# Performance work log

Measured on AMD Instinct MI355X. Metric: run time of the kernel, lower is better.

## Reference

```python
import jax, jax.numpy as jnp
import numpy as np

DIM = 1024

def setup_inputs() -> dict:
    key = jax.random.key(0)
    ks = jax.random.split(key, 7)
    s = 1.0 / np.sqrt(DIM)  # roughly match nn.Linear init scale
    return {
        "x": jax.random.normal(ks[0], (4, 2048, DIM), dtype=jnp.float32),
        "Wq": jax.random.normal(ks[1], (DIM, DIM), dtype=jnp.float32) * s,
        "bq": jax.random.normal(ks[2], (DIM,), dtype=jnp.float32) * s,
        "Wk": jax.random.normal(ks[3], (DIM, DIM), dtype=jnp.float32) * s,
        "bk": jax.random.normal(ks[4], (DIM,), dtype=jnp.float32) * s,
        "Wv": jax.random.normal(ks[5], (DIM, DIM), dtype=jnp.float32) * s,
        "bv": jax.random.normal(ks[6], (DIM,), dtype=jnp.float32) * s,
    }

def reference(x, Wq, bq, Wk, bk, Wv, bv):
    # torch Linear: y = x @ W.T + b
    C = x.shape[-1]
    scale = C ** (-0.5)
    q = jnp.einsum('bnc,dc->bnd', x, Wq) + bq
    k = jnp.einsum('bnc,dc->bnd', x, Wk) + bk
    v = jnp.einsum('bnc,dc->bnd', x, Wv) + bv
    attn = jnp.einsum('bnd,bmd->bnm', q, k) * scale  # [B,N,N]
    attn = jax.nn.softmax(attn, axis=-1)
    out = jnp.einsum('bnm,bmd->bnd', attn, v)
    return out
```

## Files before the change

kernel.cpp:

```cpp
#include <hip/hip_runtime.h>

#define SEQ  2048
#define DIM  1024
#define NTOK 8192
#define NQKV 3072

typedef __attribute__((ext_vector_type(8))) __bf16 bf16x8;
typedef __attribute__((ext_vector_type(4))) float  f32x4;

__device__ __forceinline__ unsigned short f2bf(float f) {
    unsigned int u = __float_as_uint(f);
    u += 0x7fffu + ((u >> 16) & 1u);
    return (unsigned short)(u >> 16);
}

__device__ __forceinline__ float bfu2f(unsigned int lo16) {
    return __uint_as_float(lo16 << 16);
}

__device__ __forceinline__ void load_lds_128(const unsigned short* g, unsigned short* l) {
    __builtin_amdgcn_global_load_lds(
        (const __attribute__((address_space(1))) void*)g,
        (__attribute__((address_space(3))) void*)l, 16, 0, 0);
}

#define BAR() asm volatile("s_barrier" ::: "memory")

template <int MODE>
__global__ __launch_bounds__(512, 2)
void gemm256(const unsigned short* __restrict__ A, const unsigned short* __restrict__ B,
             void* __restrict__ Cv,
             const float* __restrict__ b0v, const float* __restrict__ b1v,
             const float* __restrict__ b2v, unsigned short* __restrict__ vt,
             const float* __restrict__ inv_rs,
             int K, int lda, int ldb, int ldc,
             long sA, long sB, long sC, float alpha)
{
    constexpr int AT = 256 * 64;
    constexpr int BT = 128 * 64;
    __shared__ __align__(16) unsigned short As[3 * AT];
    __shared__ __align__(16) unsigned short Bs[3 * BT];

    const int tid  = threadIdx.x;
    const int wave = tid >> 6;
    const int lane = tid & 63;
    const int l4   = lane & 15;
    const int lh   = lane >> 4;
    const int wm   = wave >> 1;
    const int wn   = wave & 1;

    const int m0 = blockIdx.x * 256;
    const int n0 = blockIdx.y * 128;
    const int z  = blockIdx.z;
    A += (long)z * sA;
    B += (long)z * sB;

    const int r0 = tid >> 3;
    const int gc = (tid & 7) ^ (r0 & 7);
    const unsigned short* Ag = A + (long)(m0 + r0) * lda + gc * 8;
    const unsigned short* Bg = B + (long)(n0 + r0) * ldb + gc * 8;
    unsigned short* Al = As + tid * 8;
    unsigned short* Bl = Bs + tid * 8;

    const int NT = K >> 6;

    auto stage = [&](int t, int slot, int ph) {
        const long kof = (long)t * 64;
        unsigned short* al = Al + slot * AT;
        unsigned short* bl = Bl + slot * BT;
        if (ph == 0) {
            load_lds_128(Ag + kof,                          al);
            load_lds_128(Ag + kof + (long)64 * lda,         al + 4096);
            load_lds_128(Bg + kof,                          bl);
        } else {
            load_lds_128(Ag + kof + (long)128 * lda,        al + 8192);
            load_lds_128(Ag + kof + (long)192 * lda,        al + 12288);
            load_lds_128(Bg + kof + (long)64 * ldb,         bl + 4096);
        }
    };

    const int aoff = (wm * 64 + l4) * 64;
    const int boff = (wn * 64 + l4) * 64;
    const int cs0  = ((0 + lh) ^ (lane & 7)) * 8;
    const int cs1  = ((4 + lh) ^ (lane & 7)) * 8;

    f32x4 acc[4][4] = {};
    bf16x8 a0[4], b0[4], a1[4], b1[4];

    auto ldfrag = [&](bf16x8 (&a)[4], bf16x8 (&b)[4],
                      const unsigned short* Ab, const unsigned short* Bb, int cs) {
#pragma unroll
        for (int mf = 0; mf < 4; ++mf) a[mf] = *(const bf16x8*)(Ab + mf * 1024 + cs);
#pragma unroll
        for (int nf = 0; nf < 4; ++nf) b[nf] = *(const bf16x8*)(Bb + nf * 1024 + cs);
    };
    auto mfma16 = [&](bf16x8 (&a)[4], bf16x8 (&b)[4]) {
        __builtin_amdgcn_s_setprio(1);
#pragma unroll
        for (int mf = 0; mf < 4; ++mf)
#pragma unroll
            for (int nf = 0; nf < 4; ++nf)
                acc[mf][nf] = __builtin_amdgcn_mfma_f32_16x16x32_bf16(
                    a[mf], b[nf], acc[mf][nf], 0, 0, 0);
        __builtin_amdgcn_s_setprio(0);
    };

    stage(0, 0, 0); stage(0, 0, 1);
    stage(1, 1, 0); stage(1, 1, 1);
    asm volatile("s_waitcnt vmcnt(6)" ::: "memory");
    BAR();
    ldfrag(a0, b0, As + aoff, Bs + boff, cs0);

    int sl = 0;
    for (int t = 0; t < NT; ++t) {
        const unsigned short* Ab = As + sl * AT + aoff;
        const unsigned short* Bb = Bs + sl * BT + boff;
        const int st  = (sl >= 1) ? sl - 1 : 2;
        const int nsl = (sl == 2) ? 0 : sl + 1;

        ldfrag(a1, b1, Ab, Bb, cs1);
        if (t + 2 < NT) stage(t + 2, st, 0);
        mfma16(a0, b0);

        if (t + 2 < NT) stage(t + 2, st, 1);
        asm volatile("s_waitcnt lgkmcnt(0)" ::: "memory");
        if (t < NT - 2) asm volatile("s_waitcnt vmcnt(6)" ::: "memory");
        else            asm volatile("s_waitcnt vmcnt(0)" ::: "memory");
        BAR();
        if (t + 1 < NT)
            ldfrag(a0, b0, As + nsl * AT + aoff, Bs + nsl * BT + boff, cs0);
        mfma16(a1, b1);
        sl = nsl;
    }

    const int r0c = m0 + wm * 64 + lh * 4;
    const int c0c = n0 + wn * 64 + l4;

    if (MODE == 0) {
        if (n0 >= 2048) {
#pragma unroll
            for (int nf = 0; nf < 4; ++nf) {
                const int d = c0c + nf * 16 - 2048;
                const float bias = b2v[d];
#pragma unroll
                for (int mf = 0; mf < 4; ++mf) {
                    const int row = r0c + mf * 16;
                    const int bb = row >> 11;
                    const int mm = row & 2047;
                    ushort4 u;
                    u.x = f2bf(acc[mf][nf][0] + bias);
                    u.y = f2bf(acc[mf][nf][1] + bias);
                    u.z = f2bf(acc[mf][nf][2] + bias);
                    u.w = f2bf(acc[mf][nf][3] + bias);
                    *(ushort4*)(vt + ((long)bb * DIM + d) * SEQ + mm) = u;
                }
            }
        } else {
            unsigned short* C16 = (unsigned short*)Cv;
#pragma unroll
            for (int nf = 0; nf < 4; ++nf) {
                const int col = c0c + nf * 16;
                const float bias = (col >= 1024) ? b1v[col - 1024] : b0v[col];
#pragma unroll
                for (int mf = 0; mf < 4; ++mf)
#pragma unroll
                    for (int r = 0; r < 4; ++r)
                        C16[(long)(r0c + mf * 16 + r) * ldc + col] =
                            f2bf(acc[mf][nf][r] + bias);
            }
        }
    } else if (MODE == 1) {
        float* C = (float*)Cv + (long)z * sC;
        const float* ir = inv_rs + (long)z * SEQ;
#pragma unroll
        for (int mf = 0; mf < 4; ++mf) {
            const int row = r0c + mf * 16;
            const float4 inv4 = *(const float4*)(ir + row);
#pragma unroll
            for (int nf = 0; nf < 4; ++nf) {
                const int col = c0c + nf * 16;
                C[(long)(row + 0) * ldc + col] = acc[mf][nf][0] * inv4.x;
                C[(long)(row + 1) * ldc + col] = acc[mf][nf][1] * inv4.y;
                C[(long)(row + 2) * ldc + col] = acc[mf][nf][2] * inv4.z;
                C[(long)(row + 3) * ldc + col] = acc[mf][nf][3] * inv4.w;
            }
        }
    } else {
        unsigned short* C16 = (unsigned short*)Cv + (long)z * sC;
#pragma unroll
        for (int nf = 0; nf < 4; ++nf) {
            const int col = c0c + nf * 16;
#pragma unroll
            for (int mf = 0; mf < 4; ++mf)
#pragma unroll
                for (int r = 0; r < 4; ++r)
                    C16[(long)(r0c + mf * 16 + r) * ldc + col] =
                        f2bf(__expf(acc[mf][nf][r] * alpha));
        }
    }
}

__global__ __launch_bounds__(256)
void cvt_x(const float* __restrict__ src, unsigned short* __restrict__ dst, int n4)
{
    int i = blockIdx.x * 256 + threadIdx.x;
    if (i < n4) {
        float4 f = ((const float4*)src)[i];
        ushort4 u;
        u.x = f2bf(f.x); u.y = f2bf(f.y); u.z = f2bf(f.z); u.w = f2bf(f.w);
        ((ushort4*)dst)[i] = u;
    }
}

__global__ __launch_bounds__(256)
void cvt_w3(const float* __restrict__ Wq, const float* __restrict__ Wk,
            const float* __restrict__ Wv, unsigned short* __restrict__ dst)
{
    const int sel = blockIdx.y;
    const float* src = (sel == 0) ? Wq : ((sel == 1) ? Wk : Wv);
    const int i = blockIdx.x * 256 + threadIdx.x;
    float4 f = ((const float4*)src)[i];
    ushort4 u;
    u.x = f2bf(f.x); u.y = f2bf(f.y); u.z = f2bf(f.z); u.w = f2bf(f.w);
    ((ushort4*)(dst + (long)sel * DIM * DIM))[i] = u;
}

__global__ __launch_bounds__(256)
void rowsum_inv(const unsigned short* __restrict__ P, float* __restrict__ inv_rs)
{
    const int row  = blockIdx.x * 4 + (threadIdx.x >> 6);
    const int lane = threadIdx.x & 63;
    const unsigned short* pr = P + (long)row * SEQ;

    float s = 0.f;
#pragma unroll
    for (int it = 0; it < 4; ++it) {
        uint4 u = *(const uint4*)(pr + (it * 64 + lane) * 8);
        s += bfu2f(u.x & 0xffffu) + __uint_as_float(u.x & 0xffff0000u);
        s += bfu2f(u.y & 0xffffu) + __uint_as_float(u.y & 0xffff0000u);
        s += bfu2f(u.z & 0xffffu) + __uint_as_float(u.z & 0xffff0000u);
        s += bfu2f(u.w & 0xffffu) + __uint_as_float(u.w & 0xffff0000u);
    }
    for (int off = 32; off > 0; off >>= 1)
        s += __shfl_xor(s, off);
    if (lane == 0) inv_rs[row] = 1.0f / s;
}

extern "C" void kernel_launch(void* const* d_in, const int* in_sizes, int n_in,
                              void* d_out, int out_size, void* d_ws, size_t ws_size,
                              hipStream_t stream)
{
    const float* x  = (const float*)d_in[0];
    const float* Wq = (const float*)d_in[1];
    const float* bq = (const float*)d_in[2];
    const float* Wk = (const float*)d_in[3];
    const float* bk = (const float*)d_in[4];
    const float* Wv = (const float*)d_in[5];
    const float* bv = (const float*)d_in[6];
    float* out = (float*)d_out;

    char* ws = (char*)d_ws;
    unsigned short* xb   = (unsigned short*)ws;
    unsigned short* Wb   = (unsigned short*)(ws + 16u * 1024 * 1024);
    unsigned short* qkv  = (unsigned short*)(ws + 64u * 1024 * 1024);
    unsigned short* vt   = (unsigned short*)(ws + 112u * 1024 * 1024);
    unsigned short* P    = (unsigned short*)(ws + 128u * 1024 * 1024);
    float*          irs  = (float*)(ws + 160u * 1024 * 1024);

    const float scale = 0.03125f;
    dim3 blk(256);
    dim3 blk512(512);

    cvt_x<<<NTOK * DIM / 4 / 256, blk, 0, stream>>>(x, xb, NTOK * DIM / 4);
    cvt_w3<<<dim3(DIM * DIM / 4 / 256, 3), blk, 0, stream>>>(Wq, Wk, Wv, Wb);

    gemm256<0><<<dim3(NTOK / 256, NQKV / 128), blk512, 0, stream>>>(
        xb, Wb, qkv, bq, bk, bv, vt, nullptr,
        DIM, DIM, DIM, NQKV, 0, 0, 0, 1.0f);

    gemm256<2><<<dim3(SEQ / 256, SEQ / 128, 4), blk512, 0, stream>>>(
        qkv, qkv + 1024, P, nullptr, nullptr, nullptr, nullptr, nullptr,
        DIM, NQKV, NQKV, SEQ,
        (long)SEQ * NQKV, (long)SEQ * NQKV, (long)SEQ * SEQ, scale);

    rowsum_inv<<<NTOK / 4, blk, 0, stream>>>(P, irs);

    gemm256<1><<<dim3(SEQ / 256, DIM / 128, 4), blk512, 0, stream>>>(
        P, vt, out, nullptr, nullptr, nullptr, nullptr, irs,
        SEQ, SEQ, SEQ, DIM,
        (long)SEQ * SEQ, (long)DIM * SEQ, (long)SEQ * DIM, 1.0f);
}
```

Before: 244.0 us.

## Enlarge GEMM tiles to 256-wide N with 2x4 wave grid and double buffering

Replaces the 256x128 triple-buffered GEMM with a templated kernel using 256-column N tiles, a 2x4 wave layout, and a variable M tile (256 or 128). Each K-step now loads both k-halves of the fragments at once and issues the MFMAs in four quadrant groups. The aim is more operand reuse per LDS byte and fewer blocks per GEMM. In exchange, the finer-grained phased prefetch is replaced by a simple double buffer that waits for all loads every iteration. That may expose memory latency and raise register pressure.

```diff
diff --git a/kernel.cpp b/kernel.cpp
--- a/kernel.cpp
+++ b/kernel.cpp
@@ -26,31 +26,33 @@
 
 #define BAR() asm volatile("s_barrier" ::: "memory")
 
-template <int MODE>
+template <int MODE, int MB>
 __global__ __launch_bounds__(512, 2)
-void gemm256(const unsigned short* __restrict__ A, const unsigned short* __restrict__ B,
-             void* __restrict__ Cv,
-             const float* __restrict__ b0v, const float* __restrict__ b1v,
-             const float* __restrict__ b2v, unsigned short* __restrict__ vt,
-             const float* __restrict__ inv_rs,
-             int K, int lda, int ldb, int ldc,
-             long sA, long sB, long sC, float alpha)
-{
-    constexpr int AT = 256 * 64;
-    constexpr int BT = 128 * 64;
-    __shared__ __align__(16) unsigned short As[3 * AT];
-    __shared__ __align__(16) unsigned short Bs[3 * BT];
+void gemm2(const unsigned short* __restrict__ A, const unsigned short* __restrict__ B,
+           void* __restrict__ Cv,
+           const float* __restrict__ b0v, const float* __restrict__ b1v,
+           const float* __restrict__ b2v, unsigned short* __restrict__ vt,
+           const float* __restrict__ inv_rs,
+           int K, int lda, int ldb, int ldc,
+           long sA, long sB, long sC, float alpha)
+{
+    constexpr int BM = MB * 128;
+    constexpr int AT = BM * 64;
+    constexpr int BT = 256 * 64;
+    constexpr int MH = MB * 2;
+    __shared__ __align__(16) unsigned short As[2 * AT];
+    __shared__ __align__(16) unsigned short Bs[2 * BT];
 
     const int tid  = threadIdx.x;
     const int wave = tid >> 6;
     const int lane = tid & 63;
     const int l4   = lane & 15;
     const int lh   = lane >> 4;
-    const int wm   = wave >> 1;
-    const int wn   = wave & 1;
-
-    const int m0 = blockIdx.x * 256;
-    const int n0 = blockIdx.y * 128;
+    const int wm   = wave >> 2;
+    const int wn   = wave & 3;
+
+    const int m0 = blockIdx.x * BM;
+    const int n0 = blockIdx.y * 256;
     const int z  = blockIdx.z;
     A += (long)z * sA;
     B += (long)z * sB;
@@ -64,76 +66,97 @@
 
     const int NT = K >> 6;
 
-    auto stage = [&](int t, int slot, int ph) {
+    auto stage = [&](int t, int u) {
         const long kof = (long)t * 64;
-        unsigned short* al = Al + slot * AT;
-        unsigned short* bl = Bl + slot * BT;
-        if (ph == 0) {
-            load_lds_128(Ag + kof,                          al);
-            load_lds_128(Ag + kof + (long)64 * lda,         al + 4096);
-            load_lds_128(Bg + kof,                          bl);
-        } else {
-            load_lds_128(Ag + kof + (long)128 * lda,        al + 8192);
-            load_lds_128(Ag + kof + (long)192 * lda,        al + 12288);
-            load_lds_128(Bg + kof + (long)64 * ldb,         bl + 4096);
-        }
+#pragma unroll
+        for (int p = 0; p < 2 * MB; ++p)
+            load_lds_128(Ag + kof + (long)(64 * p) * lda, Al + u * AT + p * 4096);
+#pragma unroll
+        for (int p = 0; p < 4; ++p)
+            load_lds_128(Bg + kof + (long)(64 * p) * ldb, Bl + u * BT + p * 4096);
     };
 
-    const int aoff = (wm * 64 + l4) * 64;
+    const int aoff = (wm * (BM / 2) + l4) * 64;
     const int boff = (wn * 64 + l4) * 64;
     const int cs0  = ((0 + lh) ^ (lane & 7)) * 8;
     const int cs1  = ((4 + lh) ^ (lane & 7)) * 8;
 
-    f32x4 acc[4][4] = {};
-    bf16x8 a0[4], b0[4], a1[4], b1[4];
-
-    auto ldfrag = [&](bf16x8 (&a)[4], bf16x8 (&b)[4],
-                      const unsigned short* Ab, const unsigned short* Bb, int cs) {
-#pragma unroll
-        for (int mf = 0; mf < 4; ++mf) a[mf] = *(const bf16x8*)(Ab + mf * 1024 + cs);
-#pragma unroll
-        for (int nf = 0; nf < 4; ++nf) b[nf] = *(const bf16x8*)(Bb + nf * 1024 + cs);
-    };
-    auto mfma16 = [&](bf16x8 (&a)[4], bf16x8 (&b)[4]) {
+    f32x4 acc[4 * MB][4] = {};
+    bf16x8 alo[MH][2], ahi[MH][2], bfr[4][2];
+
+    stage(0, 0);
+    asm volatile("s_waitcnt vmcnt(0)" ::: "memory");
+    BAR();
+
+    for (int t = 0; t < NT; ++t) {
+        const int u = t & 1;
+        const unsigned short* Ab = As + u * AT + aoff;
+        const unsigned short* Bb = Bs + u * BT + boff;
+
+        if (t + 1 < NT) stage(t + 1, u ^ 1);
+
+#pragma unroll
+        for (int nf = 0; nf < 4; ++nf) {
+            bfr[nf][0] = *(const bf16x8*)(Bb + nf * 1024 + cs0);
+            bfr[nf][1] = *(const bf16x8*)(Bb + nf * 1024 + cs1);
+        }
+#pragma unroll
+        for (int mf = 0; mf < MH; ++mf) {
+            alo[mf][0] = *(const bf16x8*)(Ab + mf * 1024 + cs0);
+            alo[mf][1] = *(const bf16x8*)(Ab + mf * 1024 + cs1);
+        }
+#pragma unroll
+        for (int mf = 0; mf < MH; ++mf) {
+            ahi[mf][0] = *(const bf16x8*)(Ab + (MH + mf) * 1024 + cs0);
+            ahi[mf][1] = *(const bf16x8*)(Ab + (MH + mf) * 1024 + cs1);
+        }
+
         __builtin_amdgcn_s_setprio(1);
 #pragma unroll
-        for (int mf = 0; mf < 4; ++mf)
-#pragma unroll
-            for (int nf = 0; nf < 4; ++nf)
-                acc[mf][nf] = __builtin_amdgcn_mfma_f32_16x16x32_bf16(
-                    a[mf], b[nf], acc[mf][nf], 0, 0, 0);
+        for (int mf = 0; mf < MH; ++mf)
+#pragma unroll
+            for (int nf = 0; nf < 2; ++nf)
+#pragma unroll
+                for (int kk = 0; kk < 2; ++kk)
+                    acc[mf][nf] = __builtin_amdgcn_mfma_f32_16x16x32_bf16(
+                        alo[mf][kk], bfr[nf][kk], acc[mf][nf], 0, 0, 0);
         __builtin_amdgcn_s_setprio(0);
-    };
-
-    stage(0, 0, 0); stage(0, 0, 1);
-    stage(1, 1, 0); stage(1, 1, 1);
-    asm volatile("s_waitcnt vmcnt(6)" ::: "memory");
-    BAR();
-    ldfrag(a0, b0, As + aoff, Bs + boff, cs0);
-
-    int sl = 0;
-    for (int t = 0; t < NT; ++t) {
-        const unsigned short* Ab = As + sl * AT + aoff;
-        const unsigned short* Bb = Bs + sl * BT + boff;
-        const int st  = (sl >= 1) ? sl - 1 : 2;
-        const int nsl = (sl == 2) ? 0 : sl + 1;
-
-        ldfrag(a1, b1, Ab, Bb, cs1);
-        if (t + 2 < NT) stage(t + 2, st, 0);
-        mfma16(a0, b0);
-
-        if (t + 2 < NT) stage(t + 2, st, 1);
-        asm volatile("s_waitcnt lgkmcnt(0)" ::: "memory");
-        if (t < NT - 2) asm volatile("s_waitcnt vmcnt(6)" ::: "memory");
-        else            asm volatile("s_waitcnt vmcnt(0)" ::: "memory");
+        __builtin_amdgcn_s_setprio(1);
+#pragma unroll
+        for (int mf = 0; mf < MH; ++mf)
+#pragma unroll
+            for (int nf = 2; nf < 4; ++nf)
+#pragma unroll
+                for (int kk = 0; kk < 2; ++kk)
+                    acc[mf][nf] = __builtin_amdgcn_mfma_f32_16x16x32_bf16(
+                        alo[mf][kk], bfr[nf][kk], acc[mf][nf], 0, 0, 0);
+        __builtin_amdgcn_s_setprio(0);
+        __builtin_amdgcn_s_setprio(1);
+#pragma unroll
+        for (int mf = 0; mf < MH; ++mf)
+#pragma unroll
+            for (int nf = 2; nf < 4; ++nf)
+#pragma unroll
+                for (int kk = 0; kk < 2; ++kk)
+                    acc[MH + mf][nf] = __builtin_amdgcn_mfma_f32_16x16x32_bf16(
+                        ahi[mf][kk], bfr[nf][kk], acc[MH + mf][nf], 0, 0, 0);
+        __builtin_amdgcn_s_setprio(0);
+        __builtin_amdgcn_s_setprio(1);
+#pragma unroll
+        for (int mf = 0; mf < MH; ++mf)
+#pragma unroll
+            for (int nf = 0; nf < 2; ++nf)
+#pragma unroll
+                for (int kk = 0; kk < 2; ++kk)
+                    acc[MH + mf][nf] = __builtin_amdgcn_mfma_f32_16x16x32_bf16(
+                        ahi[mf][kk], bfr[nf][kk], acc[MH + mf][nf], 0, 0, 0);
+        __builtin_amdgcn_s_setprio(0);
+
+        asm volatile("s_waitcnt vmcnt(0) lgkmcnt(0)" ::: "memory");
         BAR();
-        if (t + 1 < NT)
-            ldfrag(a0, b0, As + nsl * AT + aoff, Bs + nsl * BT + boff, cs0);
-        mfma16(a1, b1);
-        sl = nsl;
     }
 
-    const int r0c = m0 + wm * 64 + lh * 4;
+    const int r0c = m0 + wm * (BM / 2) + lh * 4;
     const int c0c = n0 + wn * 64 + l4;
 
     if (MODE == 0) {
@@ -143,7 +166,7 @@
                 const int d = c0c + nf * 16 - 2048;
                 const float bias = b2v[d];
 #pragma unroll
-                for (int mf = 0; mf < 4; ++mf) {
+                for (int mf = 0; mf < 4 * MB; ++mf) {
                     const int row = r0c + mf * 16;
                     const int bb = row >> 11;
                     const int mm = row & 2047;
@@ -162,7 +185,7 @@
                 const int col = c0c + nf * 16;
                 const float bias = (col >= 1024) ? b1v[col - 1024] : b0v[col];
 #pragma unroll
-                for (int mf = 0; mf < 4; ++mf)
+                for (int mf = 0; mf < 4 * MB; ++mf)
 #pragma unroll
                     for (int r = 0; r < 4; ++r)
                         C16[(long)(r0c + mf * 16 + r) * ldc + col] =
@@ -173,7 +196,7 @@
         float* C = (float*)Cv + (long)z * sC;
         const float* ir = inv_rs + (long)z * SEQ;
 #pragma unroll
-        for (int mf = 0; mf < 4; ++mf) {
+        for (int mf = 0; mf < 4 * MB; ++mf) {
             const int row = r0c + mf * 16;
             const float4 inv4 = *(const float4*)(ir + row);
 #pragma unroll
@@ -191,7 +214,7 @@
         for (int nf = 0; nf < 4; ++nf) {
             const int col = c0c + nf * 16;
 #pragma unroll
-            for (int mf = 0; mf < 4; ++mf)
+            for (int mf = 0; mf < 4 * MB; ++mf)
 #pragma unroll
                 for (int r = 0; r < 4; ++r)
                     C16[(long)(r0c + mf * 16 + r) * ldc + col] =
@@ -274,18 +297,18 @@
     cvt_x<<<NTOK * DIM / 4 / 256, blk, 0, stream>>>(x, xb, NTOK * DIM / 4);
     cvt_w3<<<dim3(DIM * DIM / 4 / 256, 3), blk, 0, stream>>>(Wq, Wk, Wv, Wb);
 
-    gemm256<0><<<dim3(NTOK / 256, NQKV / 128), blk512, 0, stream>>>(
+    gemm2<0, 2><<<dim3(NTOK / 256, NQKV / 256), blk512, 0, stream>>>(
         xb, Wb, qkv, bq, bk, bv, vt, nullptr,
         DIM, DIM, DIM, NQKV, 0, 0, 0, 1.0f);
 
-    gemm256<2><<<dim3(SEQ / 256, SEQ / 128, 4), blk512, 0, stream>>>(
+    gemm2<2, 2><<<dim3(SEQ / 256, SEQ / 256, 4), blk512, 0, stream>>>(
         qkv, qkv + 1024, P, nullptr, nullptr, nullptr, nullptr, nullptr,
         DIM, NQKV, NQKV, SEQ,
         (long)SEQ * NQKV, (long)SEQ * NQKV, (long)SEQ * SEQ, scale);
 
     rowsum_inv<<<NTOK / 4, blk, 0, stream>>>(P, irs);
 
-    gemm256<1><<<dim3(SEQ / 256, DIM / 128, 4), blk512, 0, stream>>>(
+    gemm2<1, 1><<<dim3(SEQ / 128, DIM / 256, 4), blk512, 0, stream>>>(
         P, vt, out, nullptr, nullptr, nullptr, nullptr, irs,
         SEQ, SEQ, SEQ, DIM,
         (long)SEQ * SEQ, (long)DIM * SEQ, (long)SEQ * DIM, 1.0f);
```

Measured after the change: 272.9 us. +11.8%, slower.

## Fuse softmax row-sum into QK^T epilogue and add smaller-tile PV GEMM

Applied to the files above, without the earlier changes.

The QK^T exp epilogue now accumulates bf16-rounded row sums with shuffles and atomicAdd into a zeroed buffer. This removes the separate rowsum pass that re-read the whole P matrix. The PV product moves to a new 128x128-tile kernel with double buffering and higher occupancy, which divides by the row sum in its epilogue. The atomics add contention and an extra zeroing launch, and the smaller tiles lower reuse in exchange for more blocks.

```diff
diff --git a/kernel.cpp b/kernel.cpp
--- a/kernel.cpp
+++ b/kernel.cpp
@@ -32,7 +32,7 @@
              void* __restrict__ Cv,
              const float* __restrict__ b0v, const float* __restrict__ b1v,
              const float* __restrict__ b2v, unsigned short* __restrict__ vt,
-             const float* __restrict__ inv_rs,
+             float* __restrict__ rsv,
              int K, int lda, int ldb, int ldc,
              long sA, long sB, long sC, float alpha)
 {
@@ -169,33 +169,138 @@
                             f2bf(acc[mf][nf][r] + bias);
             }
         }
-    } else if (MODE == 1) {
-        float* C = (float*)Cv + (long)z * sC;
-        const float* ir = inv_rs + (long)z * SEQ;
-#pragma unroll
-        for (int mf = 0; mf < 4; ++mf) {
-            const int row = r0c + mf * 16;
-            const float4 inv4 = *(const float4*)(ir + row);
-#pragma unroll
-            for (int nf = 0; nf < 4; ++nf) {
-                const int col = c0c + nf * 16;
-                C[(long)(row + 0) * ldc + col] = acc[mf][nf][0] * inv4.x;
-                C[(long)(row + 1) * ldc + col] = acc[mf][nf][1] * inv4.y;
-                C[(long)(row + 2) * ldc + col] = acc[mf][nf][2] * inv4.z;
-                C[(long)(row + 3) * ldc + col] = acc[mf][nf][3] * inv4.w;
-            }
-        }
     } else {
         unsigned short* C16 = (unsigned short*)Cv + (long)z * sC;
-#pragma unroll
-        for (int nf = 0; nf < 4; ++nf) {
-            const int col = c0c + nf * 16;
-#pragma unroll
-            for (int mf = 0; mf < 4; ++mf)
-#pragma unroll
-                for (int r = 0; r < 4; ++r)
-                    C16[(long)(r0c + mf * 16 + r) * ldc + col] =
-                        f2bf(__expf(acc[mf][nf][r] * alpha));
+        float* rs = rsv + (long)z * SEQ;
+#pragma unroll
+        for (int mf = 0; mf < 4; ++mf)
+#pragma unroll
+            for (int r = 0; r < 4; ++r) {
+                const int rowi = r0c + mf * 16 + r;
+                float s = 0.f;
+#pragma unroll
+                for (int nf = 0; nf < 4; ++nf) {
+                    const int col = c0c + nf * 16;
+                    const unsigned short pu = f2bf(__expf(acc[mf][nf][r] * alpha));
+                    C16[(long)rowi * ldc + col] = pu;
+                    s += bfu2f(pu);
+                }
+                s += __shfl_xor(s, 1);
+                s += __shfl_xor(s, 2);
+                s += __shfl_xor(s, 4);
+                s += __shfl_xor(s, 8);
+                if (l4 == 0) atomicAdd(rs + rowi, s);
+            }
+    }
+}
+
+__global__ __launch_bounds__(512, 4)
+void gemm_pv(const unsigned short* __restrict__ A, const unsigned short* __restrict__ B,
+             float* __restrict__ C, const float* __restrict__ rsv,
+             int K, int lda, int ldb, int ldc, long sA, long sB, long sC)
+{
+    constexpr int AT = 128 * 64;
+    constexpr int BT = 128 * 64;
+    __shared__ __align__(16) unsigned short As[2 * AT];
+    __shared__ __align__(16) unsigned short Bs[2 * BT];
+
+    const int tid  = threadIdx.x;
+    const int wave = tid >> 6;
+    const int lane = tid & 63;
+    const int l4   = lane & 15;
+    const int lh   = lane >> 4;
+    const int wm   = wave >> 2;
+    const int wn   = wave & 3;
+
+    const int m0 = blockIdx.x * 128;
+    const int n0 = blockIdx.y * 128;
+    const int z  = blockIdx.z;
+    A += (long)z * sA;
+    B += (long)z * sB;
+
+    const int r0 = tid >> 3;
+    const int gc = (tid & 7) ^ (r0 & 7);
+    const unsigned short* Ag = A + (long)(m0 + r0) * lda + gc * 8;
+    const unsigned short* Bg = B + (long)(n0 + r0) * ldb + gc * 8;
+    unsigned short* Al = As + tid * 8;
+    unsigned short* Bl = Bs + tid * 8;
+
+    const int NT = K >> 6;
+
+    auto stage = [&](int t, int u) {
+        const long kof = (long)t * 64;
+        load_lds_128(Ag + kof,                  Al + u * AT);
+        load_lds_128(Ag + kof + (long)64 * lda, Al + u * AT + 4096);
+        load_lds_128(Bg + kof,                  Bl + u * BT);
+        load_lds_128(Bg + kof + (long)64 * ldb, Bl + u * BT + 4096);
+    };
+
+    const int aoff = (wm * 64 + l4) * 64;
+    const int boff = (wn * 32 + l4) * 64;
+    const int cs0  = (lh ^ (lane & 7)) * 8;
+    const int cs1  = ((4 + lh) ^ (lane & 7)) * 8;
+
+    f32x4 acc[4][2] = {};
+    bf16x8 aR[4][2], bR[2][2];
+
+    stage(0, 0);
+    asm volatile("s_waitcnt vmcnt(0)" ::: "memory");
+    BAR();
+
+    for (int t = 0; t < NT; ++t) {
+        const int u = t & 1;
+        const unsigned short* Ab = As + u * AT + aoff;
+        const unsigned short* Bb = Bs + u * BT + boff;
+
+        if (t + 1 < NT) stage(t + 1, u ^ 1);
+
+#pragma unroll
+        for (int mf = 0; mf < 4; ++mf) {
+            aR[mf][0] = *(const bf16x8*)(Ab + mf * 1024 + cs0);
+            aR[mf][1] = *(const bf16x8*)(Ab + mf * 1024 + cs1);
+        }
+#pragma unroll
+        for (int n = 0; n < 2; ++n) {
+            bR[n][0] = *(const bf16x8*)(Bb + n * 1024 + cs0);
+            bR[n][1] = *(const bf16x8*)(Bb + n * 1024 + cs1);
+        }
+
+        __builtin_amdgcn_s_setprio(1);
+#pragma unroll
+        for (int mf = 0; mf < 4; ++mf)
+#pragma unroll
+            for (int n = 0; n < 2; ++n)
+                acc[mf][n] = __builtin_amdgcn_mfma_f32_16x16x32_bf16(
+                    aR[mf][0], bR[n][0], acc[mf][n], 0, 0, 0);
+#pragma unroll
+        for (int mf = 0; mf < 4; ++mf)
+#pragma unroll
+            for (int n = 0; n < 2; ++n)
+                acc[mf][n] = __builtin_amdgcn_mfma_f32_16x16x32_bf16(
+                    aR[mf][1], bR[n][1], acc[mf][n], 0, 0, 0);
+        __builtin_amdgcn_s_setprio(0);
+
+        asm volatile("s_waitcnt vmcnt(0) lgkmcnt(0)" ::: "memory");
+        BAR();
+    }
+
+    float* Cz = C + (long)z * sC;
+    const float* rs = rsv + (long)z * SEQ;
+    const int r0c = m0 + wm * 64 + lh * 4;
+    const int c0c = n0 + wn * 32 + l4;
+#pragma unroll
+    for (int mf = 0; mf < 4; ++mf) {
+        const int rowb = r0c + mf * 16;
+        const float4 rs4 = *(const float4*)(rs + rowb);
+        const float i0 = 1.0f / rs4.x, i1 = 1.0f / rs4.y;
+        const float i2 = 1.0f / rs4.z, i3 = 1.0f / rs4.w;
+#pragma unroll
+        for (int n = 0; n < 2; ++n) {
+            const int col = c0c + n * 16;
+            Cz[(long)(rowb + 0) * ldc + col] = acc[mf][n][0] * i0;
+            Cz[(long)(rowb + 1) * ldc + col] = acc[mf][n][1] * i1;
+            Cz[(long)(rowb + 2) * ldc + col] = acc[mf][n][2] * i2;
+            Cz[(long)(rowb + 3) * ldc + col] = acc[mf][n][3] * i3;
         }
     }
 }
@@ -226,24 +331,9 @@
 }
 
 __global__ __launch_bounds__(256)
-void rowsum_inv(const unsigned short* __restrict__ P, float* __restrict__ inv_rs)
-{
-    const int row  = blockIdx.x * 4 + (threadIdx.x >> 6);
-    const int lane = threadIdx.x & 63;
-    const unsigned short* pr = P + (long)row * SEQ;
-
-    float s = 0.f;
-#pragma unroll
-    for (int it = 0; it < 4; ++it) {
-        uint4 u = *(const uint4*)(pr + (it * 64 + lane) * 8);
-        s += bfu2f(u.x & 0xffffu) + __uint_as_float(u.x & 0xffff0000u);
-        s += bfu2f(u.y & 0xffffu) + __uint_as_float(u.y & 0xffff0000u);
-        s += bfu2f(u.z & 0xffffu) + __uint_as_float(u.z & 0xffff0000u);
-        s += bfu2f(u.w & 0xffffu) + __uint_as_float(u.w & 0xffff0000u);
-    }
-    for (int off = 32; off > 0; off >>= 1)
-        s += __shfl_xor(s, off);
-    if (lane == 0) inv_rs[row] = 1.0f / s;
+void zero_rs(float* __restrict__ rs)
+{
+    rs[blockIdx.x * 256 + threadIdx.x] = 0.f;
 }
 
 extern "C" void kernel_launch(void* const* d_in, const int* in_sizes, int n_in,
@@ -265,7 +355,7 @@
     unsigned short* qkv  = (unsigned short*)(ws + 64u * 1024 * 1024);
     unsigned short* vt   = (unsigned short*)(ws + 112u * 1024 * 1024);
     unsigned short* P    = (unsigned short*)(ws + 128u * 1024 * 1024);
-    float*          irs  = (float*)(ws + 160u * 1024 * 1024);
+    float*          rs   = (float*)(ws + 160u * 1024 * 1024);
 
     const float scale = 0.03125f;
     dim3 blk(256);
@@ -273,20 +363,19 @@
 
     cvt_x<<<NTOK * DIM / 4 / 256, blk, 0, stream>>>(x, xb, NTOK * DIM / 4);
     cvt_w3<<<dim3(DIM * DIM / 4 / 256, 3), blk, 0, stream>>>(Wq, Wk, Wv, Wb);
+    zero_rs<<<NTOK / 256, blk, 0, stream>>>(rs);
 
     gemm256<0><<<dim3(NTOK / 256, NQKV / 128), blk512, 0, stream>>>(
         xb, Wb, qkv, bq, bk, bv, vt, nullptr,
         DIM, DIM, DIM, NQKV, 0, 0, 0, 1.0f);
 
     gemm256<2><<<dim3(SEQ / 256, SEQ / 128, 4), blk512, 0, stream>>>(
-        qkv, qkv + 1024, P, nullptr, nullptr, nullptr, nullptr, nullptr,
+        qkv, qkv + 1024, P, nullptr, nullptr, nullptr, nullptr, rs,
         DIM, NQKV, NQKV, SEQ,
         (long)SEQ * NQKV, (long)SEQ * NQKV, (long)SEQ * SEQ, scale);
 
-    rowsum_inv<<<NTOK / 4, blk, 0, stream>>>(P, irs);
-
-    gemm256<1><<<dim3(SEQ / 256, DIM / 128, 4), blk512, 0, stream>>>(
-        P, vt, out, nullptr, nullptr, nullptr, nullptr, irs,
+    gemm_pv<<<dim3(SEQ / 128, DIM / 128, 4), blk512, 0, stream>>>(
+        P, vt, out, rs,
         SEQ, SEQ, SEQ, DIM,
-        (long)SEQ * SEQ, (long)DIM * SEQ, (long)SEQ * DIM, 1.0f);
-}
+        (long)SEQ * SEQ, (long)DIM * SEQ, (long)SEQ * DIM);
+}
```

Result: slower. 249.0 us (+2.0%).

## Fuse softmax row sums into score GEMM and remap workgroups across XCDs

Applied to the files above, without the earlier changes.

The score GEMM epilogue now sums the bf16 exponentials per row with shuffles and atomically adds them into a row-sum buffer. This removes the separate rowsum pass that reread the 32 MB P matrix, and the PV GEMM takes reciprocals in its epilogue. The x and weight conversions and the zeroing of the row-sum buffer are merged into one prep launch. Workgroup IDs are also remapped so that consecutive tiles land on the same XCD, which is meant to improve L2 locality. The cost is many float atomics and a row-sum order that is no longer deterministic.

```diff
diff --git a/kernel.cpp b/kernel.cpp
--- a/kernel.cpp
+++ b/kernel.cpp
@@ -32,7 +32,7 @@
              void* __restrict__ Cv,
              const float* __restrict__ b0v, const float* __restrict__ b1v,
              const float* __restrict__ b2v, unsigned short* __restrict__ vt,
-             const float* __restrict__ inv_rs,
+             float* __restrict__ rsv,
              int K, int lda, int ldb, int ldc,
              long sA, long sB, long sC, float alpha)
 {
@@ -49,9 +49,17 @@
     const int wm   = wave >> 1;
     const int wn   = wave & 1;
 
-    const int m0 = blockIdx.x * 256;
-    const int n0 = blockIdx.y * 128;
-    const int z  = blockIdx.z;
+    const int nwg = gridDim.x * gridDim.y * gridDim.z;
+    int lin = blockIdx.x + gridDim.x * (blockIdx.y + gridDim.y * blockIdx.z);
+    lin = (lin & 7) * (nwg >> 3) + (lin >> 3);
+    const int bx = lin % gridDim.x;
+    const int t1 = lin / gridDim.x;
+    const int by = t1 % gridDim.y;
+    const int bz = t1 / gridDim.y;
+
+    const int m0 = bx * 256;
+    const int n0 = by * 128;
+    const int z  = bz;
     A += (long)z * sA;
     B += (long)z * sB;
 
@@ -171,79 +179,78 @@
         }
     } else if (MODE == 1) {
         float* C = (float*)Cv + (long)z * sC;
-        const float* ir = inv_rs + (long)z * SEQ;
+        const float* rsp = rsv + (long)z * SEQ;
 #pragma unroll
         for (int mf = 0; mf < 4; ++mf) {
-            const int row = r0c + mf * 16;
-            const float4 inv4 = *(const float4*)(ir + row);
+            const int rowb = r0c + mf * 16;
+            const float4 rs4 = *(const float4*)(rsp + rowb);
+            const float i0 = 1.0f / rs4.x, i1 = 1.0f / rs4.y;
+            const float i2 = 1.0f / rs4.z, i3 = 1.0f / rs4.w;
 #pragma unroll
             for (int nf = 0; nf < 4; ++nf) {
                 const int col = c0c + nf * 16;
-                C[(long)(row + 0) * ldc + col] = acc[mf][nf][0] * inv4.x;
-                C[(long)(row + 1) * ldc + col] = acc[mf][nf][1] * inv4.y;
-                C[(long)(row + 2) * ldc + col] = acc[mf][nf][2] * inv4.z;
-                C[(long)(row + 3) * ldc + col] = acc[mf][nf][3] * inv4.w;
+                C[(long)(rowb + 0) * ldc + col] = acc[mf][nf][0] * i0;
+                C[(long)(rowb + 1) * ldc + col] = acc[mf][nf][1] * i1;
+                C[(long)(rowb + 2) * ldc + col] = acc[mf][nf][2] * i2;
+                C[(long)(rowb + 3) * ldc + col] = acc[mf][nf][3] * i3;
             }
         }
     } else {
         unsigned short* C16 = (unsigned short*)Cv + (long)z * sC;
-#pragma unroll
-        for (int nf = 0; nf < 4; ++nf) {
-            const int col = c0c + nf * 16;
-#pragma unroll
-            for (int mf = 0; mf < 4; ++mf)
-#pragma unroll
-                for (int r = 0; r < 4; ++r)
-                    C16[(long)(r0c + mf * 16 + r) * ldc + col] =
-                        f2bf(__expf(acc[mf][nf][r] * alpha));
-        }
+        float* rs = rsv + (long)z * SEQ;
+#pragma unroll
+        for (int mf = 0; mf < 4; ++mf)
+#pragma unroll
+            for (int r = 0; r < 4; ++r) {
+                const int rowi = r0c + mf * 16 + r;
+                float s = 0.f;
+#pragma unroll
+                for (int nf = 0; nf < 4; ++nf) {
+                    const int col = c0c + nf * 16;
+                    const unsigned short pu = f2bf(__expf(acc[mf][nf][r] * alpha));
+                    C16[(long)rowi * ldc + col] = pu;
+                    s += bfu2f(pu);
+                }
+                s += __shfl_xor(s, 1);
+                s += __shfl_xor(s, 2);
+                s += __shfl_xor(s, 4);
+                s += __shfl_xor(s, 8);
+                if (l4 == 0) atomicAdd(rs + rowi, s);
+            }
     }
 }
 
+#define NX4 (NTOK * DIM / 4)
+#define NW4 (3 * DIM * DIM / 4)
+#define PREP_BLOCKS (8192 + 3072 + 32)
+
 __global__ __launch_bounds__(256)
-void cvt_x(const float* __restrict__ src, unsigned short* __restrict__ dst, int n4)
+void prep(const float* __restrict__ x,
+          const float* __restrict__ Wq, const float* __restrict__ Wk,
+          const float* __restrict__ Wv,
+          unsigned short* __restrict__ xb, unsigned short* __restrict__ Wb,
+          float* __restrict__ rs)
 {
-    int i = blockIdx.x * 256 + threadIdx.x;
-    if (i < n4) {
-        float4 f = ((const float4*)src)[i];
+    const int b = blockIdx.x;
+    if (b < 8192) {
+        const int i = b * 256 + threadIdx.x;
+        float4 f = ((const float4*)x)[i];
         ushort4 u;
         u.x = f2bf(f.x); u.y = f2bf(f.y); u.z = f2bf(f.z); u.w = f2bf(f.w);
-        ((ushort4*)dst)[i] = u;
+        ((ushort4*)xb)[i] = u;
+    } else if (b < 8192 + 3072) {
+        const int idx = (b - 8192) * 256 + threadIdx.x;
+        const int sel = idx / (DIM * DIM / 4);
+        const int j   = idx - sel * (DIM * DIM / 4);
+        const float* src = (sel == 0) ? Wq : ((sel == 1) ? Wk : Wv);
+        float4 f = ((const float4*)src)[j];
+        ushort4 u;
+        u.x = f2bf(f.x); u.y = f2bf(f.y); u.z = f2bf(f.z); u.w = f2bf(f.w);
+        ((ushort4*)(Wb + (long)sel * DIM * DIM))[j] = u;
+    } else {
+        const int idx = (b - 8192 - 3072) * 256 + threadIdx.x;
+        if (idx < NTOK) rs[idx] = 0.f;
     }
-}
-
-__global__ __launch_bounds__(256)
-void cvt_w3(const float* __restrict__ Wq, const float* __restrict__ Wk,
-            const float* __restrict__ Wv, unsigned short* __restrict__ dst)
-{
-    const int sel = blockIdx.y;
-    const float* src = (sel == 0) ? Wq : ((sel == 1) ? Wk : Wv);
-    const int i = blockIdx.x * 256 + threadIdx.x;
-    float4 f = ((const float4*)src)[i];
-    ushort4 u;
-    u.x = f2bf(f.x); u.y = f2bf(f.y); u.z = f2bf(f.z); u.w = f2bf(f.w);
-    ((ushort4*)(dst + (long)sel * DIM * DIM))[i] = u;
-}
-
-__global__ __launch_bounds__(256)
-void rowsum_inv(const unsigned short* __restrict__ P, float* __restrict__ inv_rs)
-{
-    const int row  = blockIdx.x * 4 + (threadIdx.x >> 6);
-    const int lane = threadIdx.x & 63;
-    const unsigned short* pr = P + (long)row * SEQ;
-
-    float s = 0.f;
-#pragma unroll
-    for (int it = 0; it < 4; ++it) {
-        uint4 u = *(const uint4*)(pr + (it * 64 + lane) * 8);
-        s += bfu2f(u.x & 0xffffu) + __uint_as_float(u.x & 0xffff0000u);
-        s += bfu2f(u.y & 0xffffu) + __uint_as_float(u.y & 0xffff0000u);
-        s += bfu2f(u.z & 0xffffu) + __uint_as_float(u.z & 0xffff0000u);
-        s += bfu2f(u.w & 0xffffu) + __uint_as_float(u.w & 0xffff0000u);
-    }
-    for (int off = 32; off > 0; off >>= 1)
-        s += __shfl_xor(s, off);
-    if (lane == 0) inv_rs[row] = 1.0f / s;
 }
 
 extern "C" void kernel_launch(void* const* d_in, const int* in_sizes, int n_in,
@@ -265,28 +272,24 @@
     unsigned short* qkv  = (unsigned short*)(ws + 64u * 1024 * 1024);
     unsigned short* vt   = (unsigned short*)(ws + 112u * 1024 * 1024);
     unsigned short* P    = (unsigned short*)(ws + 128u * 1024 * 1024);
-    float*          irs  = (float*)(ws + 160u * 1024 * 1024);
+    float*          rs   = (float*)(ws + 160u * 1024 * 1024);
 
     const float scale = 0.03125f;
-    dim3 blk(256);
     dim3 blk512(512);
 
-    cvt_x<<<NTOK * DIM / 4 / 256, blk, 0, stream>>>(x, xb, NTOK * DIM / 4);
-    cvt_w3<<<dim3(DIM * DIM / 4 / 256, 3), blk, 0, stream>>>(Wq, Wk, Wv, Wb);
+    prep<<<PREP_BLOCKS, 256, 0, stream>>>(x, Wq, Wk, Wv, xb, Wb, rs);
 
     gemm256<0><<<dim3(NTOK / 256, NQKV / 128), blk512, 0, stream>>>(
         xb, Wb, qkv, bq, bk, bv, vt, nullptr,
         DIM, DIM, DIM, NQKV, 0, 0, 0, 1.0f);
 
     gemm256<2><<<dim3(SEQ / 256, SEQ / 128, 4), blk512, 0, stream>>>(
-        qkv, qkv + 1024, P, nullptr, nullptr, nullptr, nullptr, nullptr,
+        qkv, qkv + 1024, P, nullptr, nullptr, nullptr, nullptr, rs,
         DIM, NQKV, NQKV, SEQ,
         (long)SEQ * NQKV, (long)SEQ * NQKV, (long)SEQ * SEQ, scale);
 
-    rowsum_inv<<<NTOK / 4, blk, 0, stream>>>(P, irs);
-
     gemm256<1><<<dim3(SEQ / 256, DIM / 128, 4), blk512, 0, stream>>>(
-        P, vt, out, nullptr, nullptr, nullptr, nullptr, irs,
+        P, vt, out, nullptr, nullptr, nullptr, nullptr, rs,
         SEQ, SEQ, SEQ, DIM,
         (long)SEQ * SEQ, (long)DIM * SEQ, (long)SEQ * DIM, 1.0f);
 }
```

After: 259.1 us. 6.2% more time.
